# Kernel tuning notes

Hardware: AMD Instinct MI355X
Metric: run time of the kernel (lower is better)

Reference implementation:

```python
import jax, jax.numpy as jnp
import numpy as np

N_NODES = 50000
N_EDGES = 800000
G_DIM = 128
H1 = 32
HEADS = 4
H2 = 64
ATT_SLOPE = 0.2   # PyG GATConv default negative_slope
LRELU_SLOPE = 0.01  # F.leaky_relu default
BN_EPS = 1e-5


def segment_softmax(logits, seg, num_segments):
    # numerically stable softmax over edges grouped by destination node
    m = jax.ops.segment_max(logits, seg, num_segments=num_segments)
    e = jnp.exp(logits - m[seg])
    s = jax.ops.segment_sum(e, seg, num_segments=num_segments)
    return e / (s[seg] + 1e-16)


def gat_layer(x, src, dst, W, a_src, a_dst, bias, concat):
    # PyG GATConv: x' = W x ; alpha_e = softmax_dst(leaky_relu(a_src.x_src + a_dst.x_dst))
    N = x.shape[0]
    H, C = a_src.shape
    xw = (x @ W).reshape(N, H, C)          # [N,H,C]
    al_s = jnp.sum(xw * a_src, axis=-1)    # [N,H]
    al_d = jnp.sum(xw * a_dst, axis=-1)    # [N,H]
    logits = jax.nn.leaky_relu(al_s[src] + al_d[dst], ATT_SLOPE)  # [E,H]
    alpha = segment_softmax(logits, dst, N)                        # [E,H]
    out = jax.ops.segment_sum(alpha[:, :, None] * xw[src], dst, num_segments=N)  # [N,H,C]
    out = out.reshape(N, H * C) if concat else out.mean(axis=1)
    return out + bias


def batchnorm_train(x, gamma, beta):
    mu = x.mean(axis=0)
    var = x.var(axis=0)  # biased, as torch BN uses for normalization
    return (x - mu) * jax.lax.rsqrt(var + BN_EPS) * gamma + beta


def setup_inputs() -> dict:
    key = jax.random.key(0)
    ks = jax.random.split(key, 12)
    node_features = jax.random.normal(ks[0], (N_NODES, G_DIM), dtype=jnp.float32)
    node_type = jax.random.randint(ks[1], (N_NODES,), 0, 3)
    edge_index = jax.random.randint(ks[2], (2, N_EDGES), 0, N_NODES)
    s1 = 1.0 / np.sqrt(G_DIM)
    s2 = 1.0 / np.sqrt(H1 * HEADS)
    return {
        "node_features": node_features,
        "node_type": node_type,
        "edge_index": edge_index,
        "W1": jax.random.normal(ks[3], (G_DIM, HEADS * H1), dtype=jnp.float32) * s1,
        "a_src1": jax.random.normal(ks[4], (HEADS, H1), dtype=jnp.float32) * s1,
        "a_dst1": jax.random.normal(ks[5], (HEADS, H1), dtype=jnp.float32) * s1,
        "b1": jnp.zeros((HEADS * H1,), dtype=jnp.float32),
        "g1": jnp.ones((HEADS * H1,), dtype=jnp.float32),
        "beta1": jnp.zeros((HEADS * H1,), dtype=jnp.float32),
        "W2": jax.random.normal(ks[6], (HEADS * H1, H2), dtype=jnp.float32) * s2,
        "a_src2": jax.random.normal(ks[7], (1, H2), dtype=jnp.float32) * s2,
        "a_dst2": jax.random.normal(ks[8], (1, H2), dtype=jnp.float32) * s2,
        "b2": jnp.zeros((H2,), dtype=jnp.float32),
        "g2": jnp.ones((H2,), dtype=jnp.float32),
        "beta2": jnp.zeros((H2,), dtype=jnp.float32),
    }


def reference(node_features, node_type, edge_index, W1, a_src1, a_dst1, b1, g1, beta1,
              W2, a_src2, a_dst2, b2, g2, beta2):
    N = node_features.shape[0]
    loop = jnp.arange(N)
    src = jnp.concatenate([edge_index[0], loop])  # add_self_loops=True (PyG default)
    dst = jnp.concatenate([edge_index[1], loop])
    x = gat_layer(node_features, src, dst, W1, a_src1, a_dst1, b1, concat=True)
    x = jax.nn.leaky_relu(batchnorm_train(x, g1, beta1), LRELU_SLOPE)
    x = gat_layer(x, src, dst, W2, a_src2, a_dst2, b2, concat=False)
    x = jax.nn.leaky_relu(batchnorm_train(x, g2, beta2), LRELU_SLOPE)
    return x
```

## Files before the change

kernel.cpp:

```cpp
#include <hip/hip_runtime.h>
#include <hip/hip_fp16.h>

#define NN 50000
#define NE 800000
#define ET 850000
#define GD 128
#define D1 128
#define NH 4
#define D2 64
#define NB_SCAN 196
#define NBP 1024
#define NXCD 8
#define NPX 6250
#define HB 4096

typedef unsigned short u16;
typedef _Float16 half8_t __attribute__((ext_vector_type(8)));
typedef float    f32x4_t __attribute__((ext_vector_type(4)));

__device__ __forceinline__ float lrelu(float x, float s) { return x > 0.f ? x : s * x; }

__global__ void k_prepw(const float* __restrict__ W1, const float* __restrict__ W2,
                        __half* __restrict__ Wp1, __half* __restrict__ Wp2,
                        int* __restrict__ cur) {
    int idx = blockIdx.x * 256 + threadIdx.x;
    if (idx < NN) cur[idx] = 0;
    if (idx < 16384) {
        int i = idx & 7, l = (idx >> 3) & 63, nt = (idx >> 9) & 7, kk = idx >> 12;
        int k = kk * 32 + (l >> 4) * 8 + i, n = nt * 16 + (l & 15);
        Wp1[idx] = __float2half(W1[k * D1 + n]);
    } else if (idx < 24576) {
        int x2 = idx - 16384;
        int i = x2 & 7, l = (x2 >> 3) & 63, nt = (x2 >> 9) & 3, kk = x2 >> 11;
        int k = kk * 32 + (l >> 4) * 8 + i, n = nt * 16 + (l & 15);
        Wp2[x2] = __float2half(W2[k * D2 + n]);
    }
}

__global__ void k_histgemm1(const int* __restrict__ ei, int* __restrict__ cnt,
                            u16* __restrict__ pos16,
                            const float* __restrict__ x, const half8_t* __restrict__ wp,
                            const float* __restrict__ as, const float* __restrict__ ad,
                            __half* __restrict__ xw, float* __restrict__ al_s,
                            float* __restrict__ al_d) {
    if (blockIdx.x < HB) {
        const int xcd = blockIdx.x & (NXCD - 1);
        const int grp = blockIdx.x >> 3;
        const int ngrp = HB >> 3;
        const int lo = xcd * NPX, hi = lo + NPX;
        for (int e = grp * 256 + threadIdx.x; e < ET; e += ngrp * 256) {
            int d = (e < NE) ? ei[NE + e] : (e - NE);
            if (d >= lo && d < hi) {
                int pos = atomicAdd(&cnt[d], 1);
                pos16[e] = (u16)pos;
            }
        }
        return;
    }
    const int strip = (blockIdx.x - HB) * 4 + (threadIdx.x >> 6);
    if (strip >= NN / 16) return;
    const int l = threadIdx.x & 63;
    const int row0 = strip * 16;
    const int c = l & 15, g = l >> 4;
    const float* xrow = x + (size_t)(row0 + c) * GD;

    f32x4_t acc[8];
#pragma unroll
    for (int nt = 0; nt < 8; nt++) acc[nt] = (f32x4_t){0.f, 0.f, 0.f, 0.f};

#pragma unroll
    for (int kk = 0; kk < 4; kk++) {
        const int koff = kk * 32 + g * 8;
        f32x4_t a0 = *(const f32x4_t*)(xrow + koff);
        f32x4_t a1 = *(const f32x4_t*)(xrow + koff + 4);
        half8_t af;
#pragma unroll
        for (int i = 0; i < 4; i++) { af[i] = (_Float16)a0[i]; af[i + 4] = (_Float16)a1[i]; }
#pragma unroll
        for (int nt = 0; nt < 8; nt++) {
            half8_t bf = wp[(kk * 8 + nt) * 64 + l];
            acc[nt] = __builtin_amdgcn_mfma_f32_16x16x32_f16(af, bf, acc[nt], 0, 0, 0);
        }
    }

    float asv[8], adv[8];
#pragma unroll
    for (int nt = 0; nt < 8; nt++) { asv[nt] = as[nt * 16 + c]; adv[nt] = ad[nt * 16 + c]; }

#pragma unroll
    for (int r = 0; r < 4; r++) {
        const int row = row0 + g * 4 + r;
        __half* xwr = xw + (size_t)row * D1;
        float hs[4] = {0.f, 0.f, 0.f, 0.f}, hd[4] = {0.f, 0.f, 0.f, 0.f};
#pragma unroll
        for (int nt = 0; nt < 8; nt++) {
            float v = acc[nt][r];
            xwr[nt * 16 + c] = __float2half(v);
            hs[nt >> 1] += v * asv[nt];
            hd[nt >> 1] += v * adv[nt];
        }
#pragma unroll
        for (int m = 1; m <= 8; m <<= 1) {
#pragma unroll
            for (int h = 0; h < 4; h++) { hs[h] += __shfl_xor(hs[h], m); hd[h] += __shfl_xor(hd[h], m); }
        }
        if (c == 0) {
#pragma unroll
            for (int h = 0; h < 4; h++) { al_s[row * NH + h] = hs[h]; al_d[row * NH + h] = hd[h]; }
        }
    }
}

__global__ void k_blocksum(const int* __restrict__ cnt, int* __restrict__ part) {
    __shared__ int r[256];
    int t = threadIdx.x, i = blockIdx.x * 256 + t;
    r[t] = (i < NN) ? cnt[i] : 0;
    __syncthreads();
    for (int s = 128; s >= 1; s >>= 1) {
        if (t < s) r[t] += r[t + s];
        __syncthreads();
    }
    if (t == 0) part[blockIdx.x] = r[0];
}

__global__ void k_scanfix(const int* __restrict__ cnt, const int* __restrict__ part,
                          int* __restrict__ row_ptr) {
    __shared__ int pp[256];
    __shared__ int r[256];
    int b = blockIdx.x, t = threadIdx.x, i = b * 256 + t;
    pp[t] = (t < NB_SCAN) ? part[t] : 0;
    int v = (i < NN) ? cnt[i] : 0;
    r[t] = v;
    __syncthreads();
    for (int off = 1; off < 256; off <<= 1) {
        int pv = (t >= off) ? pp[t - off] : 0;
        int rv = (t >= off) ? r[t - off] : 0;
        __syncthreads();
        pp[t] += pv; r[t] += rv;
        __syncthreads();
    }
    int pbase = b ? pp[b - 1] : 0;
    if (i < NN) row_ptr[i] = pbase + (t ? r[t - 1] : 0);
    if (i == NN - 1) row_ptr[NN] = pbase + r[t];
}

__global__ void k_fill_x(const int* __restrict__ ei, const int* __restrict__ row_ptr,
                         const u16* __restrict__ pos16, u16* __restrict__ csr_src) {
    const int xcd = blockIdx.x & (NXCD - 1);
    const int grp = blockIdx.x >> 3;
    const int ngrp = gridDim.x >> 3;
    const int lo = xcd * NPX, hi = lo + NPX;
    for (int e = grp * 256 + threadIdx.x; e < ET; e += ngrp * 256) {
        int d = (e < NE) ? ei[NE + e] : (e - NE);
        if (d >= lo && d < hi) {
            int s = (e < NE) ? ei[e] : d;
            csr_src[row_ptr[d] + pos16[e]] = (u16)s;
        }
    }
}

__global__ void k_gat1(const int* __restrict__ row_ptr, const u16* __restrict__ csr_src,
                       const float* __restrict__ als, const float* __restrict__ ald,
                       const __half2* __restrict__ xw, __half2* __restrict__ out) {
    const int b = blockIdx.x;
    const int d = (b & (NXCD - 1)) * NPX + (b >> 3);
    const int beg = row_ptr[d];
    const int deg = row_ptr[d + 1] - beg;
    const int lane = threadIdx.x;

    __shared__ int   s_src[64];
    __shared__ float s_al[64 * NH];

    const float4 adv = *(const float4*)(ald + d * NH);
    const int h = lane >> 4;

    float ax = 0.f, ay = 0.f, den = 0.f;
    for (int base = 0; base < deg; base += 64) {
        int cnt = min(64, deg - base);
        if (lane < cnt) {
            int s = csr_src[beg + base + lane];
            s_src[lane] = s;
            const float4 a = *(const float4*)(als + s * NH);
            s_al[lane * NH + 0] = __expf(lrelu(a.x + adv.x, 0.2f));
            s_al[lane * NH + 1] = __expf(lrelu(a.y + adv.y, 0.2f));
            s_al[lane * NH + 2] = __expf(lrelu(a.z + adv.z, 0.2f));
            s_al[lane * NH + 3] = __expf(lrelu(a.w + adv.w, 0.2f));
        }
        __syncthreads();
#pragma unroll 4
        for (int i = 0; i < cnt; i++) {
            float al = s_al[i * NH + h];
            float2 v = __half22float2(xw[(size_t)s_src[i] * 64 + lane]);
            den += al; ax += al * v.x; ay += al * v.y;
        }
        __syncthreads();
    }
    float inv = 1.f / (den + 1e-16f);
    __half2 hv;
    hv.x = __float2half(ax * inv);
    hv.y = __float2half(ay * inv);
    out[(size_t)d * 64 + lane] = hv;
}

__global__ void k_bnstats1h(const __half2* __restrict__ x, float* __restrict__ bp) {
    int t = threadIdx.x, bid = blockIdx.x;
    float s0 = 0.f, q0 = 0.f, s1 = 0.f, q1 = 0.f;
    for (int r = bid; r < NN; r += NBP) {
        float2 f = __half22float2(x[(size_t)r * 64 + t]);
        s0 += f.x; q0 += f.x * f.x;
        s1 += f.y; q1 += f.y * f.y;
    }
    bp[bid * D1 + 2 * t] = s0;
    bp[bid * D1 + 2 * t + 1] = s1;
    bp[NBP * D1 + bid * D1 + 2 * t] = q0;
    bp[NBP * D1 + bid * D1 + 2 * t + 1] = q1;
}

template <int D>
__global__ void k_bnstats(const float* __restrict__ x, float* __restrict__ bp) {
    int j = threadIdx.x, bid = blockIdx.x;
    float s = 0.f, q = 0.f;
    for (int r = bid; r < NN; r += NBP) {
        float v = x[(size_t)r * D + j];
        s += v; q += v * v;
    }
    bp[bid * D + j] = s;
    bp[NBP * D + bid * D + j] = q;
}

template <int D>
__global__ void k_bnreduce(const float* __restrict__ bp, const float* __restrict__ g,
                           const float* __restrict__ b, float* __restrict__ scale,
                           float* __restrict__ shift) {
    __shared__ float rs[256], rq[256];
    int j = blockIdx.x, t = threadIdx.x;
    float s = 0.f, q = 0.f;
    for (int i = t; i < NBP; i += 256) {
        s += bp[i * D + j];
        q += bp[NBP * D + i * D + j];
    }
    rs[t] = s; rq[t] = q;
    __syncthreads();
    for (int st = 128; st >= 1; st >>= 1) {
        if (t < st) { rs[t] += rs[t + st]; rq[t] += rq[t + st]; }
        __syncthreads();
    }
    if (t == 0) {
        float mu = rs[0] / (float)NN;
        float var = rq[0] / (float)NN - mu * mu;
        float sc = rsqrtf(var + 1e-5f) * g[j];
        scale[j] = sc;
        shift[j] = b[j] - mu * sc;
    }
}

__global__ void k_bnapply2(const float* __restrict__ x, const float* __restrict__ scale,
                           const float* __restrict__ shift, float* __restrict__ y) {
    int idx = blockIdx.x * blockDim.x + threadIdx.x;
    if (idx >= NN * D2 / 4) return;
    float4 v = ((const float4*)x)[idx];
    int c = (idx * 4) & (D2 - 1);
    v.x = lrelu(v.x * scale[c + 0] + shift[c + 0], 0.01f);
    v.y = lrelu(v.y * scale[c + 1] + shift[c + 1], 0.01f);
    v.z = lrelu(v.z * scale[c + 2] + shift[c + 2], 0.01f);
    v.w = lrelu(v.w * scale[c + 3] + shift[c + 3], 0.01f);
    ((float4*)y)[idx] = v;
}

__global__ void k_gemm2m(const __half* __restrict__ x, const float* __restrict__ scale,
                         const float* __restrict__ shift, const half8_t* __restrict__ wp,
                         const float* __restrict__ as, const float* __restrict__ ad,
                         __half* __restrict__ xw, float* __restrict__ al_s, float* __restrict__ al_d) {
    const int l = threadIdx.x;
    const int row0 = blockIdx.x * 16;
    const int c = l & 15, g = l >> 4;
    const __half* xrow = x + (size_t)(row0 + c) * D1;

    f32x4_t acc[4];
#pragma unroll
    for (int nt = 0; nt < 4; nt++) acc[nt] = (f32x4_t){0.f, 0.f, 0.f, 0.f};

#pragma unroll
    for (int kk = 0; kk < 4; kk++) {
        const int koff = kk * 32 + g * 8;
        half8_t a8 = *(const half8_t*)(xrow + koff);
        f32x4_t sc0 = *(const f32x4_t*)(scale + koff);
        f32x4_t sc1 = *(const f32x4_t*)(scale + koff + 4);
        f32x4_t sh0 = *(const f32x4_t*)(shift + koff);
        f32x4_t sh1 = *(const f32x4_t*)(shift + koff + 4);
        half8_t af;
#pragma unroll
        for (int i = 0; i < 4; i++) {
            af[i]     = (_Float16)lrelu((float)a8[i] * sc0[i] + sh0[i], 0.01f);
            af[i + 4] = (_Float16)lrelu((float)a8[i + 4] * sc1[i] + sh1[i], 0.01f);
        }
#pragma unroll
        for (int nt = 0; nt < 4; nt++) {
            half8_t bf = wp[(kk * 4 + nt) * 64 + l];
            acc[nt] = __builtin_amdgcn_mfma_f32_16x16x32_f16(af, bf, acc[nt], 0, 0, 0);
        }
    }

    float asv[4], adv[4];
#pragma unroll
    for (int nt = 0; nt < 4; nt++) { asv[nt] = as[nt * 16 + c]; adv[nt] = ad[nt * 16 + c]; }

#pragma unroll
    for (int r = 0; r < 4; r++) {
        const int row = row0 + g * 4 + r;
        __half* xwr = xw + (size_t)row * D2;
        float hs = 0.f, hd = 0.f;
#pragma unroll
        for (int nt = 0; nt < 4; nt++) {
            float v = acc[nt][r];
            xwr[nt * 16 + c] = __float2half(v);
            hs += v * asv[nt];
            hd += v * adv[nt];
        }
#pragma unroll
        for (int m = 1; m <= 8; m <<= 1) { hs += __shfl_xor(hs, m); hd += __shfl_xor(hd, m); }
        if (c == 0) { al_s[row] = hs; al_d[row] = hd; }
    }
}

__global__ void k_gat2(const int* __restrict__ row_ptr, const u16* __restrict__ csr_src,
                       const float* __restrict__ als, const float* __restrict__ ald,
                       const __half2* __restrict__ xw, float* __restrict__ out) {
    const int b = blockIdx.x;
    const int d = (b & (NXCD - 1)) * NPX + (b >> 3);
    const int beg = row_ptr[d];
    const int deg = row_ptr[d + 1] - beg;
    const int lane = threadIdx.x;
    const int sub = lane >> 5, l = lane & 31;

    const float add = ald[d];
    float ax = 0.f, ay = 0.f, den = 0.f;
    for (int base = 0; base < deg; base += 64) {
        int cnt = min(64, deg - base);
        int s = 0; float e = 0.f;
        if (lane < cnt) {
            s = csr_src[beg + base + lane];
            e = __expf(lrelu(als[s] + add, 0.2f));
        }
        int np = (cnt + 1) >> 1;
        for (int i = 0; i < np; i++) {
            int idx = 2 * i + sub;
            float al = __shfl(e, idx);
            int  si  = __shfl(s, idx);
            float2 v = __half22float2(xw[(size_t)si * 32 + l]);
            den += al; ax += al * v.x; ay += al * v.y;
        }
    }
    ax += __shfl_xor(ax, 32); ay += __shfl_xor(ay, 32); den += __shfl_xor(den, 32);
    if (lane < 32) {
        float inv = 1.f / (den + 1e-16f);
        *(float2*)(out + (size_t)d * D2 + 2 * l) = make_float2(ax * inv, ay * inv);
    }
}

extern "C" void kernel_launch(void* const* d_in, const int* in_sizes, int n_in,
                              void* d_out, int out_size, void* d_ws, size_t ws_size,
                              hipStream_t stream) {
    const float* x   = (const float*)d_in[0];
    const int*   ei  = (const int*)d_in[2];
    const float* W1  = (const float*)d_in[3];
    const float* as1 = (const float*)d_in[4];
    const float* ad1 = (const float*)d_in[5];
    const float* g1  = (const float*)d_in[7];
    const float* be1 = (const float*)d_in[8];
    const float* W2  = (const float*)d_in[9];
    const float* as2 = (const float*)d_in[10];
    const float* ad2 = (const float*)d_in[11];
    const float* g2  = (const float*)d_in[13];
    const float* be2 = (const float*)d_in[14];
    float* out = (float*)d_out;

    float* ws = (float*)d_ws;
    __half* xw1  = (__half*)ws;
    __half* xw2  = (__half*)ws;
    float* bp    = ws + 1600000;
    float* al_s2 = ws + 3200000;
    float* al_d2 = ws + 3250000;
    float* al_s1 = ws + 6400000;
    float* al_d1 = al_s1 + 200000;
    __half* agg1 = (__half*)(al_d1 + 200000);
    u16*   pos16 = (u16*)agg1;
    float* aggE  = al_d1 + 200000 + 6400000;
    int*   row_ptr = (int*)aggE;
    int*   cur     = row_ptr + 50001;
    int*   part    = cur + 50000;
    float* st      = (float*)(part + 199);
    u16*   csr_src = (u16*)(st + 768);
    __half* Wp1    = (__half*)(csr_src + 850000);
    __half* Wp2    = Wp1 + 16384;

    k_prepw<<<196, 256, 0, stream>>>(W1, W2, Wp1, Wp2, cur);
    k_histgemm1<<<HB + (NN / 16 + 3) / 4, 256, 0, stream>>>(ei, cur, pos16, x,
                                                            (const half8_t*)Wp1,
                                                            as1, ad1, xw1, al_s1, al_d1);
    k_blocksum<<<NB_SCAN, 256, 0, stream>>>(cur, part);
    k_scanfix<<<NB_SCAN, 256, 0, stream>>>(cur, part, row_ptr);
    k_fill_x<<<4096, 256, 0, stream>>>(ei, row_ptr, pos16, csr_src);

    k_gat1<<<NN, 64, 0, stream>>>(row_ptr, csr_src, al_s1, al_d1, (const __half2*)xw1,
                                  (__half2*)agg1);
    k_bnstats1h<<<NBP, 64, 0, stream>>>((const __half2*)agg1, bp);
    k_bnreduce<D1><<<D1, 256, 0, stream>>>(bp, g1, be1, st, st + 128);

    k_gemm2m<<<NN / 16, 64, 0, stream>>>(agg1, st, st + 128, (const half8_t*)Wp2, as2, ad2,
                                         xw2, al_s2, al_d2);
    k_gat2<<<NN, 64, 0, stream>>>(row_ptr, csr_src, al_s2, al_d2, (const __half2*)xw2, out);
    k_bnstats<D2><<<NBP, D2, 0, stream>>>(out, bp);
    k_bnreduce<D2><<<D2, 256, 0, stream>>>(bp, g2, be2, st + 256, st + 320);
    k_bnapply2<<<(NN * D2 / 4 + 255) / 256, 256, 0, stream>>>(out, st + 256, st + 320, out);
}
```

Baseline: 194.9 us.

## Pad histogram counters to 64 bytes and drop XCD-partitioned edge loop

Degree counters now sit one per 64-byte line (stride 16 ints), and the histogram phase runs one edge per thread instead of each XCD group scanning every edge and keeping only the destinations in its own node range. The padding is meant to stop atomics on neighbouring counters from contending on the same cache line, and the flat loop avoids reading the edge list eight times. The cost is that atomics from all XCDs now land on any counter, and the scan kernels read counters with a strided pattern. Workspace offsets are reshuffled to make room for the padded array.

```diff
diff --git a/kernel.cpp b/kernel.cpp
--- a/kernel.cpp
+++ b/kernel.cpp
@@ -12,7 +12,7 @@
 #define NBP 1024
 #define NXCD 8
 #define NPX 6250
-#define HB 4096
+#define HB 3321
 
 typedef unsigned short u16;
 typedef _Float16 half8_t __attribute__((ext_vector_type(8)));
@@ -22,9 +22,9 @@
 
 __global__ void k_prepw(const float* __restrict__ W1, const float* __restrict__ W2,
                         __half* __restrict__ Wp1, __half* __restrict__ Wp2,
-                        int* __restrict__ cur) {
+                        int* __restrict__ cnt16) {
     int idx = blockIdx.x * 256 + threadIdx.x;
-    if (idx < NN) cur[idx] = 0;
+    if (idx < NN) cnt16[idx * 16] = 0;
     if (idx < 16384) {
         int i = idx & 7, l = (idx >> 3) & 63, nt = (idx >> 9) & 7, kk = idx >> 12;
         int k = kk * 32 + (l >> 4) * 8 + i, n = nt * 16 + (l & 15);
@@ -37,23 +37,18 @@
     }
 }
 
-__global__ void k_histgemm1(const int* __restrict__ ei, int* __restrict__ cnt,
+__global__ void k_histgemm1(const int* __restrict__ ei, int* __restrict__ cnt16,
                             u16* __restrict__ pos16,
                             const float* __restrict__ x, const half8_t* __restrict__ wp,
                             const float* __restrict__ as, const float* __restrict__ ad,
                             __half* __restrict__ xw, float* __restrict__ al_s,
                             float* __restrict__ al_d) {
     if (blockIdx.x < HB) {
-        const int xcd = blockIdx.x & (NXCD - 1);
-        const int grp = blockIdx.x >> 3;
-        const int ngrp = HB >> 3;
-        const int lo = xcd * NPX, hi = lo + NPX;
-        for (int e = grp * 256 + threadIdx.x; e < ET; e += ngrp * 256) {
+        int e = blockIdx.x * 256 + threadIdx.x;
+        if (e < ET) {
             int d = (e < NE) ? ei[NE + e] : (e - NE);
-            if (d >= lo && d < hi) {
-                int pos = atomicAdd(&cnt[d], 1);
-                pos16[e] = (u16)pos;
-            }
+            int pos = atomicAdd(&cnt16[d * 16], 1);
+            pos16[e] = (u16)pos;
         }
         return;
     }
@@ -111,10 +106,10 @@
     }
 }
 
-__global__ void k_blocksum(const int* __restrict__ cnt, int* __restrict__ part) {
+__global__ void k_blocksum(const int* __restrict__ cnt16, int* __restrict__ part) {
     __shared__ int r[256];
     int t = threadIdx.x, i = blockIdx.x * 256 + t;
-    r[t] = (i < NN) ? cnt[i] : 0;
+    r[t] = (i < NN) ? cnt16[i * 16] : 0;
     __syncthreads();
     for (int s = 128; s >= 1; s >>= 1) {
         if (t < s) r[t] += r[t + s];
@@ -123,13 +118,13 @@
     if (t == 0) part[blockIdx.x] = r[0];
 }
 
-__global__ void k_scanfix(const int* __restrict__ cnt, const int* __restrict__ part,
+__global__ void k_scanfix(const int* __restrict__ cnt16, const int* __restrict__ part,
                           int* __restrict__ row_ptr) {
     __shared__ int pp[256];
     __shared__ int r[256];
     int b = blockIdx.x, t = threadIdx.x, i = b * 256 + t;
     pp[t] = (t < NB_SCAN) ? part[t] : 0;
-    int v = (i < NN) ? cnt[i] : 0;
+    int v = (i < NN) ? cnt16[i * 16] : 0;
     r[t] = v;
     __syncthreads();
     for (int off = 1; off < 256; off <<= 1) {
@@ -383,23 +378,25 @@
     float* al_d2 = ws + 3250000;
     float* al_s1 = ws + 6400000;
     float* al_d1 = al_s1 + 200000;
-    __half* agg1 = (__half*)(al_d1 + 200000);
-    u16*   pos16 = (u16*)agg1;
-    float* aggE  = al_d1 + 200000 + 6400000;
-    int*   row_ptr = (int*)aggE;
-    int*   cur     = row_ptr + 50001;
-    int*   part    = cur + 50000;
-    float* st      = (float*)(part + 199);
+    float* aggF  = al_d1 + 200000;
+    __half* agg1 = (__half*)aggF;
+    u16*   pos16 = (u16*)aggF;
+    int*   cnt16 = (int*)(aggF + 425008);
+    float* aggE  = aggF + 6400000 / 2 * 2;
+    int*   row_ptr = (int*)(al_d1 + 200000 + 6400000);
+    int*   part    = row_ptr + 50001;
+    float* st      = (float*)(part + 249);
     u16*   csr_src = (u16*)(st + 768);
     __half* Wp1    = (__half*)(csr_src + 850000);
     __half* Wp2    = Wp1 + 16384;
-
-    k_prepw<<<196, 256, 0, stream>>>(W1, W2, Wp1, Wp2, cur);
-    k_histgemm1<<<HB + (NN / 16 + 3) / 4, 256, 0, stream>>>(ei, cur, pos16, x,
+    (void)aggE;
+
+    k_prepw<<<196, 256, 0, stream>>>(W1, W2, Wp1, Wp2, cnt16);
+    k_histgemm1<<<HB + (NN / 16 + 3) / 4, 256, 0, stream>>>(ei, cnt16, pos16, x,
                                                             (const half8_t*)Wp1,
                                                             as1, ad1, xw1, al_s1, al_d1);
-    k_blocksum<<<NB_SCAN, 256, 0, stream>>>(cur, part);
-    k_scanfix<<<NB_SCAN, 256, 0, stream>>>(cur, part, row_ptr);
+    k_blocksum<<<NB_SCAN, 256, 0, stream>>>(cnt16, part);
+    k_scanfix<<<NB_SCAN, 256, 0, stream>>>(cnt16, part, row_ptr);
     k_fill_x<<<4096, 256, 0, stream>>>(ei, row_ptr, pos16, csr_src);
 
     k_gat1<<<NN, 64, 0, stream>>>(row_ptr, csr_src, al_s1, al_d1, (const __half2*)xw1,
```

Measured after the change: 197.6 us. About the same (+1.3%).
